# Kernel tuning notes

Measured on AMD Instinct MI355X. Metric: run time of the kernel, lower is better.

## Reference

```python
import jax, jax.numpy as jnp
import numpy as np

B, N = 16384, 31
N_INTS, N_OPS, N_PASSES = 10, 4, 4
NODE_LIT, NODE_OP = 0, 1


def setup_inputs() -> dict:
    key = jax.random.key(0)
    ks = jax.random.split(key, 7)
    cats = jax.random.randint(ks[0], (B, N), 0, 2)
    ops = jax.random.randint(ks[1], (B, N), 0, N_OPS)
    lits = jax.random.randint(ks[2], (B, N), 0, N_INTS)
    left = jax.random.randint(ks[3], (B, N), 0, N)
    right = jax.random.randint(ks[4], (B, N), 0, N)
    mask = jnp.ones((B, N), dtype=bool)
    op_table = jax.random.normal(ks[5], (N_OPS, N_INTS, N_INTS, N_INTS), dtype=jnp.float32) * 0.1
    return {"cats": cats, "ops": ops, "lits": lits, "left": left,
            "right": right, "mask": mask, "op_table": op_table}


def reference(cats, ops, lits, left, right, mask, op_table):
    left = jnp.clip(left, 0, N - 1)
    right = jnp.clip(right, 0, N - 1)
    ops_c = jnp.clip(ops, 0, N_OPS - 1)

    # init: literals -> one-hot over ints, everything else zero
    lit_mask = (cats == NODE_LIT) & mask                     # (B, N)
    lit_onehot = jax.nn.one_hot(jnp.clip(lits, 0, N_INTS - 1), N_INTS, dtype=jnp.float32)
    state = jnp.where(lit_mask[..., None], lit_onehot, 0.0)  # (B, N, n_ints)

    op_mask = (cats == NODE_OP) & mask
    brow = jnp.arange(B)[:, None]
    slice_table = op_table[ops_c]                             # (B, N, i, j, k)

    def op_step(state):
        left_dist = state[brow, left]                         # (B, N, n_ints)
        right_dist = state[brow, right]                       # (B, N, n_ints)
        logits = jnp.einsum('bni,bnj,bnijk->bnk', left_dist, right_dist, slice_table)
        dist = jax.nn.softmax(logits, axis=-1)
        new_state = jnp.where(op_mask[..., None], dist, state)
        return new_state, logits

    for _ in range(N_PASSES - 1):
        state, _ = op_step(state)
    state, node_logits = op_step(state)

    root_is_lit = (cats[:, 0] == NODE_LIT)[:, None].astype(jnp.float32)
    lit_logits = state[:, 0, :] * 10.0
    root_logits = root_is_lit * lit_logits + (1.0 - root_is_lit) * node_logits[:, 0, :]
    return root_logits
```

## Files before the change

### kernel.cpp

```cpp
#include <hip/hip_runtime.h>

#define NB 16384
#define NN 31
#define NI 10
#define NOPS 4
#define GB 64
#define TPB 1024
#define NWAVES 16
#define NPB (GB * NN)
#define ZSLOT (NPB + 10)
#define NROWS (NPB + 11)
#define NDR_TOT 1200
#define MAXT_PW 3
#define INVALID_NODE 0xFFFFu

typedef __attribute__((ext_vector_type(8))) short bf16x8_t;
typedef __attribute__((ext_vector_type(4))) float f32x4_t;

template <int CTRL>
__device__ __forceinline__ float dppf(float v) {
    return __int_as_float(__builtin_amdgcn_update_dpp(
        0, __float_as_int(v), CTRL, 0xF, 0xF, true));
}
__device__ __forceinline__ float rowsum16(float x) {
    x += dppf<0xB1>(x);
    x += dppf<0x4E>(x);
    x += dppf<0x124>(x);
    x += dppf<0x128>(x);
    return x;
}
__device__ __forceinline__ unsigned short f2bf(float f) {
    unsigned u = __float_as_uint(f);
    u += 0x7FFFu + ((u >> 16) & 1u);
    return (unsigned short)(u >> 16);
}
__device__ __forceinline__ unsigned cvtpk(float lo, float hi) {
    unsigned r;
    asm("v_cvt_pk_bf16_f32 %0, %1, %2" : "=v"(r) : "v"(lo), "v"(hi));
    return r;
}
__device__ __forceinline__ int ndrOff(int p) {
    return (p == 0) ? 0 : (p == 1) ? 572 : (p == 2) ? 888 : 1076;
}

__global__ __launch_bounds__(TPB, 4) void listops_mfma(
    const int* __restrict__ cats, const int* __restrict__ ops,
    const int* __restrict__ lits, const int* __restrict__ left,
    const int* __restrict__ right, const float* __restrict__ tbl,
    float* __restrict__ out)
{
    __shared__ __align__(16) float st[NROWS][12];
    __shared__ __align__(16) unsigned short Bl[NOPS * 4 * 64 * 8];
    __shared__ unsigned chLR[NPB];
    __shared__ unsigned short chIdx[NPB];
    __shared__ unsigned short slotOf[NPB];
    __shared__ unsigned opm[GB];
    __shared__ unsigned Mfr[4][GB];
    __shared__ unsigned short ndr[NDR_TOT];
    __shared__ int cntA[16], cntB[16], baseA[16], ntP[4];
    __shared__ unsigned char tOpA[4][36];

    const int tid = threadIdx.x;
    const int wv  = tid >> 6;
    const int l   = tid & 63;
    const int q   = l >> 4;
    const int c   = l & 15;

    const int g0 = blockIdx.x * NPB + tid;
    const bool v1 = (tid + TPB) < NPB;
    const int g1 = v1 ? (g0 + TPB) : g0;
    int cat0 = cats[g0], opv0 = ops[g0], lit0 = lits[g0], lf0 = left[g0], rt0 = right[g0];
    int cat1 = cats[g1], opv1 = ops[g1], lit1 = lits[g1], lf1 = left[g1], rt1 = right[g1];
    float4 tv = make_float4(0.f, 0.f, 0.f, 0.f);
    if (tid < 1000) tv = ((const float4*)tbl)[tid];

    float* tscr = &st[0][0];
    if (tid < 16) { cntA[tid] = 0; cntB[tid] = 0; }
    if (tid < GB) { opm[tid] = 0u; Mfr[0][tid] = 0u; Mfr[1][tid] = 0u; Mfr[2][tid] = 0u; }
    ndr[tid] = (unsigned short)INVALID_NODE;
    if (tid < NDR_TOT - TPB) ndr[TPB + tid] = (unsigned short)INVALID_NODE;
    if (tid < 132) {
        int r = tid / 12, k = tid - r * 12;
        st[NPB + r][k] = (r < NI && k == r) ? 1.0f : 0.0f;
    }
    if (tid < 1000) ((float4*)tscr)[tid] = tv;
    __syncthreads();

    {
        const int fi   = tid;
        const int lane = fi & 63;
        const int step = (fi >> 6) & 3;
        const int op   = fi >> 8;
        const int bq = lane >> 4, bn = lane & 15;
        unsigned short v[8];
        #pragma unroll
        for (int e = 0; e < 8; ++e) {
            float val = 0.0f;
            if (bn < NI) {
                if (step < 2) {
                    val = tscr[((op * NI + 4 * step + bq) * NI + e) * NI + bn];
                } else if (step == 2) {
                    if (bq < 2) val = tscr[((op * NI + 8 + bq) * NI + e) * NI + bn];
                } else {
                    if (bq < 2)      val = tscr[((op * NI + e) * NI + 8 + bq) * NI + bn];
                    else if (e < 2)  val = tscr[((op * NI + 8 + e) * NI + 8 + (bq - 2)) * NI + bn];
                }
            }
            v[e] = f2bf(val);
        }
        uint4 pk;
        pk.x = (unsigned)v[0] | ((unsigned)v[1] << 16);
        pk.y = (unsigned)v[2] | ((unsigned)v[3] << 16);
        pk.z = (unsigned)v[4] | ((unsigned)v[5] << 16);
        pk.w = (unsigned)v[6] | ((unsigned)v[7] << 16);
        ((uint4*)&Bl[0])[fi] = pk;
    }
    int myOp0 = 0, myCl0 = 0, myCr0 = 0;
    {
        int n = tid;
        int b  = n / NN, nl = n - b * NN;
        myOp0 = min(max(opv0, 0), NOPS - 1);
        int lit = min(max(lit0, 0), NI - 1);
        myCl0 = min(max(lf0, 0), NN - 1);
        myCr0 = min(max(rt0, 0), NN - 1);
        chIdx[n]  = (unsigned short)(myCl0 | (myCr0 << 5) | (myOp0 << 10));
        slotOf[n] = (unsigned short)((cat0 == 0) ? (NPB + lit) : n);
        if (cat0 == 0) {
            if (nl == 0) {
                float* o = out + (blockIdx.x * GB + b) * NI;
                #pragma unroll
                for (int k = 0; k < NI; ++k) o[k] = (k == lit) ? 10.0f : 0.0f;
            }
        } else {
            atomicOr(&opm[b], 1u << nl);
        }
        if (v1) {
            n = tid + TPB;
            b = n / NN; nl = n - b * NN;
            int op  = min(max(opv1, 0), NOPS - 1);
            int li  = min(max(lit1, 0), NI - 1);
            int cl  = min(max(lf1, 0), NN - 1);
            int cr  = min(max(rt1, 0), NN - 1);
            chIdx[n]  = (unsigned short)(cl | (cr << 5) | (op << 10));
            slotOf[n] = (unsigned short)((cat1 == 0) ? (NPB + li) : n);
            if (cat1 == 0) {
                if (nl == 0) {
                    float* o = out + (blockIdx.x * GB + b) * NI;
                    #pragma unroll
                    for (int k = 0; k < NI; ++k) o[k] = (k == li) ? 10.0f : 0.0f;
                }
            } else {
                atomicOr(&opm[b], 1u << nl);
            }
        }
    }
    __syncthreads();

    #pragma unroll
    for (int rr = 0; rr < 2; ++rr) {
        int n = tid + rr * TPB;
        if (n < NPB) {
            int b = n / NN;
            unsigned ch = chIdx[n];
            unsigned sl = slotOf[b * NN + (ch & 31)];
            unsigned sr = slotOf[b * NN + ((ch >> 5) & 31)];
            chLR[n] = (sl * 3u) | ((sr * 3u) << 16);
        }
    }
    {
        int b = tid / NN, nl = tid - (tid / NN) * NN;
        if (nl == 0) {
            unsigned isop = opm[b] & 1u;
            Mfr[3][b] = isop;
            if (isop) {
                atomicOr(&Mfr[2][b], (1u << myCl0) | (1u << myCr0));
                atomicAdd(&cntA[12 + myOp0], 1);
            }
        }
        if (v1) {
            int n = tid + TPB;
            int b2 = n / NN, nl2 = n - b2 * NN;
            if (nl2 == 0) {
                unsigned isop = opm[b2] & 1u;
                Mfr[3][b2] = isop;
                if (isop) {
                    unsigned ch = chIdx[n];
                    atomicOr(&Mfr[2][b2], (1u << (ch & 31)) | (1u << ((ch >> 5) & 31)));
                    atomicAdd(&cntA[12 + ((ch >> 10) & 3)], 1);
                }
            }
        }
    }
    __syncthreads();

    #pragma unroll
    for (int p = 2; p >= 1; --p) {
        #pragma unroll
        for (int rr = 0; rr < 2; ++rr) {
            int n = tid + rr * TPB;
            if (n < NPB) {
                int b  = n / NN;
                int nl = n - b * NN;
                if (((opm[b] >> nl) & 1u) && ((Mfr[p][b] >> nl) & 1u)) {
                    unsigned ch = chIdx[n];
                    atomicOr(&Mfr[p - 1][b], (1u << (ch & 31)) | (1u << ((ch >> 5) & 31)));
                    atomicAdd(&cntA[p * 4 + ((ch >> 10) & 3)], 1);
                }
            }
        }
        __syncthreads();
    }
    #pragma unroll
    for (int rr = 0; rr < 2; ++rr) {
        int n = tid + rr * TPB;
        if (n < NPB) {
            int b  = n / NN;
            int nl = n - b * NN;
            if (((opm[b] >> nl) & 1u) && ((Mfr[0][b] >> nl) & 1u))
                atomicAdd(&cntA[(chIdx[n] >> 10) & 3], 1);
        }
    }
    __syncthreads();

    if (tid < 16) {
        int p = tid >> 2, o = tid & 3;
        int nt0 = (cntA[p * 4 + 0] + 15) >> 4;
        int nt1 = (cntA[p * 4 + 1] + 15) >> 4;
        int nt2 = (cntA[p * 4 + 2] + 15) >> 4;
        int nt3 = (cntA[p * 4 + 3] + 15) >> 4;
        int myNt = (o == 0) ? nt0 : (o == 1) ? nt1 : (o == 2) ? nt2 : nt3;
        int tb = ((o > 0) ? nt0 : 0) + ((o > 1) ? nt1 : 0) + ((o > 2) ? nt2 : 0);
        baseA[p * 4 + o] = tb << 4;
        for (int i = 0; i < myNt; ++i) tOpA[p][tb + i] = (unsigned char)o;
        if (o == 3) ntP[p] = tb + nt3;
    }
    __syncthreads();

    #pragma unroll
    for (int rr = 0; rr < 2; ++rr) {
        int n = tid + rr * TPB;
        if (n < NPB) {
            int b  = n / NN;
            int nl = n - b * NN;
            if ((opm[b] >> nl) & 1u) {
                int o = (chIdx[n] >> 10) & 3;
                #pragma unroll
                for (int p = 0; p < 4; ++p) {
                    if ((Mfr[p][b] >> nl) & 1u) {
                        int r = atomicAdd(&cntB[p * 4 + o], 1);
                        ndr[ndrOff(p) + baseA[p * 4 + o] + r] =
                            (unsigned short)((b << 5) | nl);
                    }
                }
            }
        }
    }
    __syncthreads();

    const char* sb = (const char*)&st[0][0];
    #pragma unroll 1
    for (int pass = 0; pass < 4; ++pass) {
        const unsigned short* nd = &ndr[ndrOff(pass)];
        const unsigned char* top = &tOpA[pass][0];
        const int nt = ntP[pass];
        f32x4_t acc[MAXT_PW];

        #pragma unroll
        for (int i = 0; i < MAXT_PW; ++i) {
            int t = wv + NWAVES * i;
            if (t < nt) {
                int rowv = nd[t * 16 + c];
                int idx  = (rowv == (int)INVALID_NODE) ? 0
                         : ((rowv >> 5) * NN + (rowv & 31));
                unsigned lrp = chLR[idx];
                if (pass == 0) {
                    unsigned lo = lrp & 0xFFFFu, hi = lrp >> 16;
                    lo = (lo < 3u * NPB) ? (3u * ZSLOT) : lo;
                    hi = (hi < 3u * NPB) ? (3u * ZSLOT) : hi;
                    lrp = lo | (hi << 16);
                }
                const char* Lb = sb + ((lrp & 0xFFFFu) << 4);
                const char* Rb = sb + ((lrp >> 16) << 4);
                float4 l0  = *(const float4*)Lb;
                float4 l1  = *(const float4*)(Lb + 16);
                float2 l89 = *(const float2*)(Lb + 32);
                float4 r0  = *(const float4*)Rb;
                float4 r1  = *(const float4*)(Rb + 16);
                float2 r89 = *(const float2*)(Rb + 32);

                float lq0 = (q & 2) ? ((q & 1) ? l0.w : l0.z) : ((q & 1) ? l0.y : l0.x);
                float lq1 = (q & 2) ? ((q & 1) ? l1.w : l1.z) : ((q & 1) ? l1.y : l1.x);
                float lq2 = (q == 0) ? l89.x : ((q == 1) ? l89.y : 0.0f);

                float Re[8] = {r0.x, r0.y, r0.z, r0.w, r1.x, r1.y, r1.z, r1.w};
                float Le[8] = {l0.x, l0.y, l0.z, l0.w, l1.x, l1.y, l1.z, l1.w};

                bf16x8_t av0, av1, av2, av3;
                unsigned* a0 = (unsigned*)&av0;
                unsigned* a1 = (unsigned*)&av1;
                unsigned* a2 = (unsigned*)&av2;
                unsigned* a3 = (unsigned*)&av3;
                float rsel = (q & 1) ? r89.y : r89.x;
                const bool qlo = (q < 2);
                float w3[8];
                w3[0] = (qlo ? Le[0] : l89.x) * rsel;
                w3[1] = (qlo ? Le[1] : l89.y) * rsel;
                #pragma unroll
                for (int e = 2; e < 8; ++e) w3[e] = (qlo ? Le[e] : 0.0f) * rsel;
                #pragma unroll
                for (int d = 0; d < 4; ++d) {
                    a0[d] = cvtpk(lq0 * Re[2 * d], lq0 * Re[2 * d + 1]);
                    a1[d] = cvtpk(lq1 * Re[2 * d], lq1 * Re[2 * d + 1]);
                    a2[d] = cvtpk(lq2 * Re[2 * d], lq2 * Re[2 * d + 1]);
                    a3[d] = cvtpk(w3[2 * d], w3[2 * d + 1]);
                }

                const char* Bp = (const char*)&Bl[0] + (int)top[t] * 4096 + l * 16;
                f32x4_t a = {0.0f, 0.0f, 0.0f, 0.0f};
                a = __builtin_amdgcn_mfma_f32_16x16x32_bf16(av0, *(const bf16x8_t*)(Bp + 0 * 1024), a, 0, 0, 0);
                a = __builtin_amdgcn_mfma_f32_16x16x32_bf16(av1, *(const bf16x8_t*)(Bp + 1 * 1024), a, 0, 0, 0);
                a = __builtin_amdgcn_mfma_f32_16x16x32_bf16(av2, *(const bf16x8_t*)(Bp + 2 * 1024), a, 0, 0, 0);
                a = __builtin_amdgcn_mfma_f32_16x16x32_bf16(av3, *(const bf16x8_t*)(Bp + 3 * 1024), a, 0, 0, 0);
                acc[i] = a;
            }
        }
        __syncthreads();

        if (pass < 3) {
            #pragma unroll
            for (int i = 0; i < MAXT_PW; ++i) {
                int t = wv + NWAVES * i;
                if (t < nt) {
                    f32x4_t a = acc[i];
                    ushort4 nds = *(const ushort4*)&nd[t * 16 + 4 * q];
                    const unsigned short* np = (const unsigned short*)&nds;
                    #pragma unroll
                    for (int r = 0; r < 4; ++r) {
                        float ex = (c < NI) ? __expf(a[r]) : 0.0f;
                        float sd = rowsum16(ex);
                        float pv = ex * __builtin_amdgcn_rcpf(sd);
                        unsigned short ndv = np[r];
                        if (ndv != (unsigned short)INVALID_NODE && c < NI) {
                            int i2 = ((int)ndv >> 5) * NN + ((int)ndv & 31);
                            st[i2][c] = pv;
                        }
                    }
                }
            }
            __syncthreads();
        } else {
            #pragma unroll
            for (int i = 0; i < MAXT_PW; ++i) {
                int t = wv + NWAVES * i;
                if (t < nt) {
                    f32x4_t a = acc[i];
                    ushort4 nds = *(const ushort4*)&nd[t * 16 + 4 * q];
                    const unsigned short* np = (const unsigned short*)&nds;
                    #pragma unroll
                    for (int r = 0; r < 4; ++r) {
                        unsigned short ndv = np[r];
                        if (ndv != (unsigned short)INVALID_NODE && c < NI) {
                            int b = (int)ndv >> 5;
                            out[(blockIdx.x * GB + b) * NI + c] = a[r];
                        }
                    }
                }
            }
        }
    }
}

extern "C" void kernel_launch(void* const* d_in, const int* in_sizes, int n_in,
                              void* d_out, int out_size, void* d_ws, size_t ws_size,
                              hipStream_t stream) {
    const int*   cats     = (const int*)  d_in[0];
    const int*   ops      = (const int*)  d_in[1];
    const int*   lits     = (const int*)  d_in[2];
    const int*   left     = (const int*)  d_in[3];
    const int*   right    = (const int*)  d_in[4];
    const float* op_table = (const float*)d_in[6];
    float*       out      = (float*)      d_out;

    hipLaunchKernelGGL(listops_mfma, dim3(NB / GB), dim3(TPB), 0, stream,
                       cats, ops, lits, left, right, op_table, out);
}
```

Measured before the change: 15.20 us.

## Halve block size to 32 batches and merge last frontier pass

Shrinks each block from 64 to 32 batch rows (512 threads, 8 waves), which doubles the grid and reshapes the per-pass node offsets and table-staging loops to match the smaller block. The last frontier-propagation step is folded into the previous one: newly set bits from an atomicOr are counted immediately, which removes one barrier. The barrier after the final MFMA pass is also skipped. The goal is better occupancy and load balance and fewer syncs, at the cost of more blocks each loading the op table and a serial loop inside the merged pass.

```diff
diff --git a/kernel.cpp b/kernel.cpp
--- a/kernel.cpp
+++ b/kernel.cpp
@@ -4,13 +4,13 @@
 #define NN 31
 #define NI 10
 #define NOPS 4
-#define GB 64
-#define TPB 1024
-#define NWAVES 16
+#define GB 32
+#define TPB 512
+#define NWAVES 8
 #define NPB (GB * NN)
 #define ZSLOT (NPB + 10)
 #define NROWS (NPB + 11)
-#define NDR_TOT 1200
+#define NDR_TOT 672
 #define MAXT_PW 3
 #define INVALID_NODE 0xFFFFu
 
@@ -40,10 +40,10 @@
     return r;
 }
 __device__ __forceinline__ int ndrOff(int p) {
-    return (p == 0) ? 0 : (p == 1) ? 572 : (p == 2) ? 888 : 1076;
-}
-
-__global__ __launch_bounds__(TPB, 4) void listops_mfma(
+    return (p == 0) ? 0 : (p == 1) ? 304 : (p == 2) ? 480 : 592;
+}
+
+__global__ __launch_bounds__(TPB, 2) void listops_mfma(
     const int* __restrict__ cats, const int* __restrict__ ops,
     const int* __restrict__ lits, const int* __restrict__ left,
     const int* __restrict__ right, const float* __restrict__ tbl,
@@ -58,7 +58,7 @@
     __shared__ unsigned Mfr[4][GB];
     __shared__ unsigned short ndr[NDR_TOT];
     __shared__ int cntA[16], cntB[16], baseA[16], ntP[4];
-    __shared__ unsigned char tOpA[4][36];
+    __shared__ unsigned char tOpA[4][20];
 
     const int tid = threadIdx.x;
     const int wv  = tid >> 6;
@@ -67,12 +67,14 @@
     const int c   = l & 15;
 
     const int g0 = blockIdx.x * NPB + tid;
-    const bool v1 = (tid + TPB) < NPB;
+    const bool v1 = tid < (NPB - TPB);
     const int g1 = v1 ? (g0 + TPB) : g0;
     int cat0 = cats[g0], opv0 = ops[g0], lit0 = lits[g0], lf0 = left[g0], rt0 = right[g0];
     int cat1 = cats[g1], opv1 = ops[g1], lit1 = lits[g1], lf1 = left[g1], rt1 = right[g1];
-    float4 tv = make_float4(0.f, 0.f, 0.f, 0.f);
-    if (tid < 1000) tv = ((const float4*)tbl)[tid];
+    float4 tv0 = make_float4(0.f, 0.f, 0.f, 0.f);
+    float4 tv1 = make_float4(0.f, 0.f, 0.f, 0.f);
+    tv0 = ((const float4*)tbl)[tid < 1000 ? tid : 0];
+    if (tid < 488) tv1 = ((const float4*)tbl)[tid + 512];
 
     float* tscr = &st[0][0];
     if (tid < 16) { cntA[tid] = 0; cntB[tid] = 0; }
@@ -83,11 +85,13 @@
         int r = tid / 12, k = tid - r * 12;
         st[NPB + r][k] = (r < NI && k == r) ? 1.0f : 0.0f;
     }
-    if (tid < 1000) ((float4*)tscr)[tid] = tv;
-    __syncthreads();
-
-    {
-        const int fi   = tid;
+    if (tid < 1000) ((float4*)tscr)[tid] = tv0;
+    if (tid < 488)  ((float4*)tscr)[tid + 512] = tv1;
+    __syncthreads();
+
+    #pragma unroll
+    for (int rr = 0; rr < 2; ++rr) {
+        const int fi   = tid + rr * TPB;
         const int lane = fi & 63;
         const int step = (fi >> 6) & 3;
         const int op   = fi >> 8;
@@ -194,30 +198,36 @@
     __syncthreads();
 
     #pragma unroll
-    for (int p = 2; p >= 1; --p) {
-        #pragma unroll
-        for (int rr = 0; rr < 2; ++rr) {
-            int n = tid + rr * TPB;
-            if (n < NPB) {
-                int b  = n / NN;
-                int nl = n - b * NN;
-                if (((opm[b] >> nl) & 1u) && ((Mfr[p][b] >> nl) & 1u)) {
-                    unsigned ch = chIdx[n];
-                    atomicOr(&Mfr[p - 1][b], (1u << (ch & 31)) | (1u << ((ch >> 5) & 31)));
-                    atomicAdd(&cntA[p * 4 + ((ch >> 10) & 3)], 1);
-                }
-            }
-        }
-        __syncthreads();
-    }
-    #pragma unroll
     for (int rr = 0; rr < 2; ++rr) {
         int n = tid + rr * TPB;
         if (n < NPB) {
             int b  = n / NN;
             int nl = n - b * NN;
-            if (((opm[b] >> nl) & 1u) && ((Mfr[0][b] >> nl) & 1u))
-                atomicAdd(&cntA[(chIdx[n] >> 10) & 3], 1);
+            if (((opm[b] >> nl) & 1u) && ((Mfr[2][b] >> nl) & 1u)) {
+                unsigned ch = chIdx[n];
+                atomicOr(&Mfr[1][b], (1u << (ch & 31)) | (1u << ((ch >> 5) & 31)));
+                atomicAdd(&cntA[8 + ((ch >> 10) & 3)], 1);
+            }
+        }
+    }
+    __syncthreads();
+    #pragma unroll
+    for (int rr = 0; rr < 2; ++rr) {
+        int n = tid + rr * TPB;
+        if (n < NPB) {
+            int b  = n / NN;
+            int nl = n - b * NN;
+            if (((opm[b] >> nl) & 1u) && ((Mfr[1][b] >> nl) & 1u)) {
+                unsigned ch = chIdx[n];
+                unsigned bits = (1u << (ch & 31)) | (1u << ((ch >> 5) & 31));
+                unsigned old  = atomicOr(&Mfr[0][b], bits);
+                atomicAdd(&cntA[4 + ((ch >> 10) & 3)], 1);
+                unsigned nw = bits & ~old & opm[b];
+                while (nw) {
+                    int chn = __builtin_ctz(nw); nw &= nw - 1;
+                    atomicAdd(&cntA[(chIdx[b * NN + chn] >> 10) & 3], 1);
+                }
+            }
         }
     }
     __syncthreads();
@@ -324,9 +334,9 @@
                 acc[i] = a;
             }
         }
-        __syncthreads();
 
         if (pass < 3) {
+            __syncthreads();
             #pragma unroll
             for (int i = 0; i < MAXT_PW; ++i) {
                 int t = wv + NWAVES * i;
```

After: 16.55 us. 8.9% more time.
